# Kernel tuning notes

Hardware: AMD Instinct MI355X
Metric: run time of the kernel (lower is better)

## Reference

```python
import jax, jax.numpy as jnp
import numpy as np

N = 512
NODE_IN = 64
NODE_OUT = 64
ED_IN = 32
ED_OUT = 32
STATE = 80  # must satisfy 2*NODE_IN + ED_IN == 2*STATE
SLOPE = 0.1
EPS = 1e-5


def setup_inputs() -> dict:
    key = jax.random.key(0)
    ks = jax.random.split(key, 10)
    def lin(k, out_f, in_f):
        return jax.random.normal(k, (out_f, in_f), jnp.float32) / np.sqrt(in_f).astype(np.float32)
    x = jax.random.normal(ks[0], (N, NODE_IN), jnp.float32)
    edge_attr = jax.random.normal(ks[1], (N * N, ED_IN), jnp.float32)
    mask = jax.random.randint(ks[2], (N * N, 1), 0, 2).astype(jnp.int32)
    return {
        "x": x,
        "edge_attr": edge_attr,
        "mask": mask,
        "W_nu": lin(ks[3], NODE_OUT, NODE_IN),
        "b_nu": jnp.zeros((NODE_OUT,), jnp.float32),
        "W_h2": lin(ks[4], STATE, 2 * STATE),
        "b_h2": jnp.zeros((STATE,), jnp.float32),
        "W_eo": lin(ks[5], ED_OUT, STATE),
        "b_eo": jnp.zeros((ED_OUT,), jnp.float32),
        "e_vec": jax.random.normal(ks[6], (2 * NODE_OUT + ED_OUT,), jnp.float32) * 0.1,
        "bn_n_w": jnp.ones((NODE_OUT,), jnp.float32),
        "bn_n_b": jnp.zeros((NODE_OUT,), jnp.float32),
        "bn_e_w": jnp.ones((ED_OUT,), jnp.float32),
        "bn_e_b": jnp.zeros((ED_OUT,), jnp.float32),
    }


def _lrelu(v):
    return jax.nn.leaky_relu(v, SLOPE)


def _bn(v, w, b):
    # BatchNorm1d, training-mode (batch stats, biased variance)
    mu = v.mean(axis=0)
    var = v.var(axis=0)
    return (v - mu) / jnp.sqrt(var + EPS) * w + b


def reference(x, edge_attr, mask, W_nu, b_nu, W_h2, b_h2, W_eo, b_eo, e_vec,
              bn_n_w, bn_n_b, bn_e_w, bn_e_b):
    n = x.shape[0]
    m = mask.astype(x.dtype)  # [N*N, 1]
    # triplet_e[i*N+j] = [x_i, edge_attr_{ij}, x_j]
    src = jnp.repeat(x, n, axis=0)          # [N*N, NODE_IN]
    dst = jnp.tile(x, (n, 1))               # [N*N, NODE_IN]
    triplet_e = jnp.concatenate([src, edge_attr, dst], axis=-1)  # [N*N, 2*STATE]
    # NOTE: ed_trans_layer / ed_hidden_1 outputs are dead code in the source.
    h = _lrelu(triplet_e @ W_h2.T + b_h2)                 # [N*N, STATE]
    new_edge_attr = _lrelu(h @ W_eo.T + b_eo)             # [N*N, ED_OUT]
    new_edge_attr = new_edge_attr * m
    xn = _lrelu(x @ W_nu.T + b_nu)                        # [N, NODE_OUT]
    triplet_n = jnp.concatenate(
        [jnp.repeat(xn, n, axis=0), new_edge_attr, jnp.tile(xn, (n, 1))], axis=-1
    ).reshape(n, n, 2 * NODE_OUT + ED_OUT)
    scores = _lrelu(jnp.einsum("ijd,d->ij", triplet_n, e_vec))  # [N, N]
    att = jax.nn.softmax(scores, axis=1)
    att = (att.reshape(n * n, 1) * m).reshape(n, n)
    # dropout disabled (deterministic / eval)
    new_x = att @ xn                                       # [N, NODE_OUT]
    new_x = _bn(new_x, bn_n_w, bn_n_b)
    new_edge_attr = _bn(new_edge_attr, bn_e_w, bn_e_b)
    return new_x, new_edge_attr
```

## Files before the change

### kernel.cpp

```cpp
#include <hip/hip_runtime.h>

#define SLOPE 0.1f
#define EPS 1e-5f

typedef __bf16 bf16x8 __attribute__((ext_vector_type(8)));
typedef unsigned short u16x8 __attribute__((ext_vector_type(8)));
typedef float f32x4 __attribute__((ext_vector_type(4)));
typedef unsigned u32x4 __attribute__((ext_vector_type(4)));

#define WS_ESC 0
#define WS_ESH 32
#define WS_A 64
#define WS_B 576
#define WS_XN 1088
#define WS_NEWX 33856
#define WS_P1B 66624
#define WS_SC 107584
#define WS_PART 369728
#define WSH_WB 804992
#define WSH_WB2 810112
#define WSH_WO 812672
#define WSH_XB 815744
#define WSH_NE 848512

__device__ __forceinline__ float lrelu(float v) { return v > 0.f ? v : SLOPE * v; }
__device__ __forceinline__ unsigned short f2bf(float f) {
  unsigned x = __float_as_uint(f);
  return (unsigned short)((x + 0x7fffu + ((x >> 16) & 1u)) >> 16);
}
__device__ __forceinline__ float bf2f(unsigned short u) {
  return __uint_as_float(((unsigned)u) << 16);
}

__global__ void __launch_bounds__(256) k1(const float* __restrict__ x,
                                          const float* __restrict__ W_nu,
                                          const float* __restrict__ b_nu,
                                          const float* __restrict__ W_h2,
                                          const float* __restrict__ b_h2,
                                          const float* __restrict__ W_eo,
                                          const float* __restrict__ ev,
                                          float* ws) {
  int blk = blockIdx.x;
  int tid = threadIdx.x;
  unsigned short* wsh = (unsigned short*)ws;
  if (blk < 128) {
    __shared__ float wlds[64 * 65];
#pragma unroll
    for (int it = 0; it < 16; it++) {
      int idx = it * 256 + tid;
      wlds[(idx >> 6) * 65 + (idx & 63)] = W_nu[idx];
    }
    int gid = blk * 256 + tid;
    wsh[WSH_XB + gid] = f2bf(x[gid]);
    ws[WS_PART + gid] = 0.f;
    if (gid < 5120) {
      int c = gid / 2560, r = gid - c * 2560;
      int t = r >> 9, l = (r >> 3) & 63, jj = r & 7;
      int n = t * 16 + (l & 15);
      int k = (l >> 4) * 8 + jj + c * 32;
      wsh[WSH_WB + gid] = f2bf(W_h2[n * 160 + 64 + k]);
    } else if (gid < 7680) {
      int idx = gid - 5120;
      int t = idx >> 9, l = (idx >> 3) & 63, jj = idx & 7;
      int n = t * 16 + (l & 15);
      int k = (l >> 4) * 8 + jj;
      wsh[WSH_WB2 + idx] = f2bf(W_h2[n * 160 + 128 + k]);
    } else if (gid < 10752) {
      int idx = gid - 7680;
      int t2 = idx / 1536, r2 = idx - t2 * 1536;
      int s = r2 >> 9, l = (r2 >> 3) & 63, jj = r2 & 7;
      int n = t2 * 16 + (l & 15);
      int k = s * 32 + (l >> 4) * 8 + jj;
      wsh[WSH_WO + idx] = (k < 80) ? f2bf(W_eo[n * 80 + k]) : (unsigned short)0;
    }
    __syncthreads();
    int i = blk * 4 + (tid >> 6);
    int c = tid & 63;
    float acc = b_nu[c];
    const float* xr = x + i * 64;
#pragma unroll 8
    for (int k = 0; k < 64; k++) acc += xr[k] * wlds[c * 65 + k];
    float xnv = lrelu(acc);
    ws[WS_XN + i * 64 + c] = xnv;
    float va = xnv * ev[c];
    float vb = xnv * ev[96 + c];
#pragma unroll
    for (int off = 32; off >= 1; off >>= 1) {
      va += __shfl_xor(va, off, 64);
      vb += __shfl_xor(vb, off, 64);
    }
    if (c == 0) { ws[WS_A + i] = va; ws[WS_B + i] = vb; }
  } else {
    int b2 = blk - 128;
    int bm = b2 & 7, bn = b2 >> 3;
    int wave = tid >> 6, lane = tid & 63;
    int c16 = lane & 15, q = lane >> 4;
    int n = bn * 16 + c16;
    const float* wrow = W_h2 + n * 160;
    int mrow = bm * 64 + wave * 16 + c16;
    bf16x8 bfr[2], afr[2];
#pragma unroll
    for (int ks = 0; ks < 2; ks++) {
      const float* bs = wrow + ks * 32 + q * 8;
      const float* as = x + mrow * 64 + ks * 32 + q * 8;
      u16x8 ub, ua;
#pragma unroll
      for (int jj = 0; jj < 8; jj++) { ub[jj] = f2bf(bs[jj]); ua[jj] = f2bf(as[jj]); }
      bfr[ks] = __builtin_bit_cast(bf16x8, ub);
      afr[ks] = __builtin_bit_cast(bf16x8, ua);
    }
    float bias = b_h2[n];
    f32x4 acc = {bias, bias, bias, bias};
    acc = __builtin_amdgcn_mfma_f32_16x16x32_bf16(afr[0], bfr[0], acc, 0, 0, 0);
    acc = __builtin_amdgcn_mfma_f32_16x16x32_bf16(afr[1], bfr[1], acc, 0, 0, 0);
#pragma unroll
    for (int r = 0; r < 4; r++) {
      int mm = bm * 64 + wave * 16 + q * 4 + r;
      ws[WS_P1B + mm * 80 + n] = acc[r];
    }
  }
}

__global__ void __launch_bounds__(256) k2(const float* __restrict__ ea,
                                          const int* __restrict__ mask,
                                          const float* __restrict__ b_eo,
                                          const float* __restrict__ ev,
                                          float* ws) {
  __shared__ unsigned short wlds[10752];
  __shared__ unsigned short ht[64 * 104];
  __shared__ float p1s[80];
  __shared__ float wred[2][4][32];
  int tid = threadIdx.x;
  int w = tid >> 6, lane = tid & 63;
  int c16 = lane & 15, q = lane >> 4;
  int blk = blockIdx.x;
  int i = blk >> 3, j0 = (blk & 7) << 6;
  int jb = j0 + w * 16;
  const unsigned short* wsh = (const unsigned short*)ws;
  unsigned* ne32 = (unsigned*)((unsigned short*)ws + WSH_NE);

#pragma unroll
  for (int it = 0; it < 6; it++) {
    int idx = it * 256 + tid;
    if (idx < 1344) *(u16x8*)&wlds[idx * 8] = *(const u16x8*)(wsh + WSH_WB + idx * 8);
  }
  if (tid < 80) p1s[tid] = ws[WS_P1B + i * 80 + tid];
  float beo0 = b_eo[c16], beo1 = b_eo[16 + c16];
  float eve0 = ev[64 + c16], eve1 = ev[80 + c16];
  float a_i = ws[WS_A + i];
  __syncthreads();

  bf16x8 af0;
  {
    const float* src = ea + (i * 512 + jb + c16) * 32 + q * 8;
    u16x8 u;
#pragma unroll
    for (int jj = 0; jj < 8; jj++) u[jj] = f2bf(src[jj]);
    af0 = __builtin_bit_cast(bf16x8, u);
  }
  bf16x8 af1 = __builtin_bit_cast(
      bf16x8, *(const u16x8*)(wsh + WSH_XB + (jb + c16) * 64 + q * 8));
  bf16x8 af2 = __builtin_bit_cast(
      bf16x8, *(const u16x8*)(wsh + WSH_XB + (jb + c16) * 64 + 32 + q * 8));

  f32x4 acc[5];
#pragma unroll
  for (int t = 0; t < 5; t++) {
    float p1v = p1s[t * 16 + c16];
    acc[t] = {p1v, p1v, p1v, p1v};
  }
#pragma unroll
  for (int t = 0; t < 5; t++) {
    bf16x8 wb = __builtin_bit_cast(bf16x8, *(const u16x8*)&wlds[t * 512 + lane * 8]);
    acc[t] = __builtin_amdgcn_mfma_f32_16x16x32_bf16(af0, wb, acc[t], 0, 0, 0);
  }
#pragma unroll
  for (int t = 0; t < 5; t++) {
    bf16x8 wb =
        __builtin_bit_cast(bf16x8, *(const u16x8*)&wlds[2560 + t * 512 + lane * 8]);
    acc[t] = __builtin_amdgcn_mfma_f32_16x16x32_bf16(af1, wb, acc[t], 0, 0, 0);
  }
#pragma unroll
  for (int t = 0; t < 5; t++) {
    bf16x8 wb =
        __builtin_bit_cast(bf16x8, *(const u16x8*)&wlds[5120 + t * 512 + lane * 8]);
    acc[t] = __builtin_amdgcn_mfma_f32_16x16x32_bf16(af2, wb, acc[t], 0, 0, 0);
  }
#pragma unroll
  for (int t = 0; t < 5; t++)
#pragma unroll
    for (int r = 0; r < 4; r++)
      ht[(w * 16 + q * 4 + r) * 104 + t * 16 + c16] = f2bf(lrelu(acc[t][r]));

  f32x4 acc2[2] = {{0.f, 0.f, 0.f, 0.f}, {0.f, 0.f, 0.f, 0.f}};
  int hrow = w * 16 + c16;
#pragma unroll
  for (int s = 0; s < 3; s++) {
    int kk = s * 32 + q * 8;
    u16x8 hb = {0, 0, 0, 0, 0, 0, 0, 0};
    if (kk < 80) hb = *(const u16x8*)&ht[hrow * 104 + kk];
    bf16x8 ha = __builtin_bit_cast(bf16x8, hb);
    bf16x8 wo0 =
        __builtin_bit_cast(bf16x8, *(const u16x8*)&wlds[7680 + s * 512 + lane * 8]);
    bf16x8 wo1 = __builtin_bit_cast(
        bf16x8, *(const u16x8*)&wlds[7680 + 1536 + s * 512 + lane * 8]);
    acc2[0] = __builtin_amdgcn_mfma_f32_16x16x32_bf16(ha, wo0, acc2[0], 0, 0, 0);
    acc2[1] = __builtin_amdgcn_mfma_f32_16x16x32_bf16(ha, wo1, acc2[1], 0, 0, 0);
  }

  float scs0 = 0.f, scss0 = 0.f, scs1 = 0.f, scss1 = 0.f;
  float se[4];
#pragma unroll
  for (int r = 0; r < 4; r++) {
    int m = i * 512 + jb + q * 4 + r;
    float mf = mask[m] ? 1.f : 0.f;
    float v0 = lrelu(acc2[0][r] + beo0) * mf;
    float v1 = lrelu(acc2[1][r] + beo1) * mf;
    scs0 += v0; scss0 += v0 * v0;
    scs1 += v1; scss1 += v1 * v1;
    ne32[m * 16 + c16] = (unsigned)f2bf(v0) | ((unsigned)f2bf(v1) << 16);
    float s = v0 * eve0 + v1 * eve1;
#pragma unroll
    for (int off = 8; off >= 1; off >>= 1) s += __shfl_xor(s, off, 64);
    se[r] = s;
  }
  if (c16 < 4) {
    int j = jb + q * 4 + c16;
    float s = (c16 == 0) ? se[0] : (c16 == 1) ? se[1] : (c16 == 2) ? se[2] : se[3];
    ws[WS_SC + i * 512 + j] = lrelu(a_i + ws[WS_B + j] + s);
  }
  scs0 += __shfl_xor(scs0, 16, 64); scs0 += __shfl_xor(scs0, 32, 64);
  scss0 += __shfl_xor(scss0, 16, 64); scss0 += __shfl_xor(scss0, 32, 64);
  scs1 += __shfl_xor(scs1, 16, 64); scs1 += __shfl_xor(scs1, 32, 64);
  scss1 += __shfl_xor(scss1, 16, 64); scss1 += __shfl_xor(scss1, 32, 64);
  if (q == 0) {
    wred[0][w][c16] = scs0; wred[0][w][16 + c16] = scs1;
    wred[1][w][c16] = scss0; wred[1][w][16 + c16] = scss1;
  }
  __syncthreads();
  if (tid < 64) {
    int half = tid >> 5, col = tid & 31;
    float v = wred[half][0][col] + wred[half][1][col] + wred[half][2][col] +
              wred[half][3][col];
    atomicAdd(&ws[WS_PART + (blk >> 3) * 64 + tid], v);
  }
}

__global__ void __launch_bounds__(512) k3(const int* __restrict__ mask,
                                          const float* __restrict__ bn_e_w,
                                          const float* __restrict__ bn_e_b,
                                          float* ws) {
  __shared__ float att[512];
  __shared__ float red[8];
  __shared__ float nx[8][64];
  int i = blockIdx.x, tid = threadIdx.x;
  int wave = tid >> 6, lane = tid & 63;
  if (i == 512) {
    int g = tid >> 6, c = tid & 63;
    float a = 0.f;
    for (int s = g; s < 512; s += 8) a += ws[WS_PART + s * 64 + c];
    nx[g][c] = a;
    __syncthreads();
    if (tid < 64) {
      float t = 0.f;
#pragma unroll
      for (int g2 = 0; g2 < 8; g2++) t += nx[g2][tid];
      att[tid] = t;
    }
    __syncthreads();
    if (tid < 32) {
      float mean = att[tid] * (1.f / 262144.f);
      float var = att[tid + 32] * (1.f / 262144.f) - mean * mean;
      float s = bn_e_w[tid] * rsqrtf(fmaxf(var, 0.f) + EPS);
      ws[WS_ESC + tid] = s;
      ws[WS_ESH + tid] = bn_e_b[tid] - mean * s;
    }
    return;
  }
  float p = __expf(ws[WS_SC + i * 512 + tid]);
  float sm = p;
#pragma unroll
  for (int off = 32; off >= 1; off >>= 1) sm += __shfl_xor(sm, off, 64);
  if (lane == 0) red[wave] = sm;
  __syncthreads();
  float tot = red[0] + red[1] + red[2] + red[3] + red[4] + red[5] + red[6] + red[7];
  att[tid] = p * (1.f / tot) * (mask[i * 512 + tid] ? 1.f : 0.f);
  __syncthreads();
  int c = lane;
  const float* xn = ws + WS_XN;
  float accv = 0.f;
#pragma unroll 4
  for (int u = 0; u < 64; u++) {
    int j = wave * 64 + u;
    accv += att[j] * xn[j * 64 + c];
  }
  nx[wave][c] = accv;
  __syncthreads();
  if (tid < 64) {
    float s = 0.f;
#pragma unroll
    for (int w = 0; w < 8; w++) s += nx[w][tid];
    ws[WS_NEWX + i * 64 + tid] = s;
  }
}

__global__ void __launch_bounds__(256) k5(const float* __restrict__ bn_n_w,
                                          const float* __restrict__ bn_n_b,
                                          const float* __restrict__ ws,
                                          float* __restrict__ out) {
  int blk = blockIdx.x, tid = threadIdx.x;
  if (blk < 8) {
    __shared__ float s1[4][64], s2[4][64], scl[64], sh[64];
    int c = tid & 63, g = tid >> 6;
    float a = 0.f, b = 0.f;
#pragma unroll 4
    for (int u = 0; u < 128; u++) {
      float v = ws[WS_NEWX + (g * 128 + u) * 64 + c];
      a += v;
      b += v * v;
    }
    s1[g][c] = a;
    s2[g][c] = b;
    __syncthreads();
    if (tid < 64) {
      float sum = s1[0][tid] + s1[1][tid] + s1[2][tid] + s1[3][tid];
      float ssq = s2[0][tid] + s2[1][tid] + s2[2][tid] + s2[3][tid];
      float mean = sum * (1.f / 512.f);
      float var = ssq * (1.f / 512.f) - mean * mean;
      float s = bn_n_w[tid] * rsqrtf(fmaxf(var, 0.f) + EPS);
      scl[tid] = s;
      sh[tid] = bn_n_b[tid] - mean * s;
    }
    __syncthreads();
#pragma unroll 4
    for (int u = 0; u < 16; u++) {
      int idx = blk * 4096 + u * 256 + tid;
      int c2 = idx & 63;
      out[idx] = ws[WS_NEWX + idx] * scl[c2] + sh[c2];
    }
  } else {
    const unsigned* ne32 = (const unsigned*)((const unsigned short*)ws + WSH_NE);
    int b4 = ((blk - 8) * 256 + tid) * 4;
    u32x4 raw = *(const u32x4*)(ne32 + b4);
    int e32 = (b4 >> 4) * 32;
    int cb = b4 & 15;
    f32x4 esc0 = *(const f32x4*)(ws + WS_ESC + cb);
    f32x4 esc1 = *(const f32x4*)(ws + WS_ESC + 16 + cb);
    f32x4 esh0 = *(const f32x4*)(ws + WS_ESH + cb);
    f32x4 esh1 = *(const f32x4*)(ws + WS_ESH + 16 + cb);
    f32x4 lo, hi;
#pragma unroll
    for (int u = 0; u < 4; u++) {
      lo[u] = bf2f((unsigned short)(raw[u] & 0xffffu)) * esc0[u] + esh0[u];
      hi[u] = bf2f((unsigned short)(raw[u] >> 16)) * esc1[u] + esh1[u];
    }
    float* oe = out + 32768;
    *(f32x4*)(oe + e32 + cb) = lo;
    *(f32x4*)(oe + e32 + 16 + cb) = hi;
  }
}

extern "C" void kernel_launch(void* const* d_in, const int* in_sizes, int n_in,
                              void* d_out, int out_size, void* d_ws, size_t ws_size,
                              hipStream_t stream) {
  const float* x = (const float*)d_in[0];
  const float* ea = (const float*)d_in[1];
  const int* mask = (const int*)d_in[2];
  const float* Wnu = (const float*)d_in[3];
  const float* bnu = (const float*)d_in[4];
  const float* Wh2 = (const float*)d_in[5];
  const float* bh2 = (const float*)d_in[6];
  const float* Weo = (const float*)d_in[7];
  const float* beo = (const float*)d_in[8];
  const float* ev = (const float*)d_in[9];
  const float* bnw = (const float*)d_in[10];
  const float* bnb = (const float*)d_in[11];
  const float* bew = (const float*)d_in[12];
  const float* beb = (const float*)d_in[13];
  float* ws = (float*)d_ws;
  float* out = (float*)d_out;

  k1<<<168, 256, 0, stream>>>(x, Wnu, bnu, Wh2, bh2, Weo, ev, ws);
  k2<<<4096, 256, 0, stream>>>(ea, mask, beo, ev, ws);
  k3<<<513, 512, 0, stream>>>(mask, bew, beb, ws);
  k5<<<4104, 256, 0, stream>>>(bnw, bnb, ws, out);
}
```

Measured before the change: 159.9 us.

## Fuse edge BatchNorm output into attention kernel and vectorize edge/mask loads

Moves the edge BatchNorm statistics finalization and the normalized-edge write from the separate stats block and the 4096 extra k5 blocks into every k3 block. Each k3 block now redundantly reduces the partial sums and then writes its own row of normalized edge attributes, which leaves k5 handling only node BN. In k2, the edge_attr and mask loads become vector loads. The cost is redundant reduction work in each of 512 blocks, traded for fewer blocks and cheaper edge-path memory access.

```diff
diff --git a/kernel.cpp b/kernel.cpp
--- a/kernel.cpp
+++ b/kernel.cpp
@@ -153,15 +153,20 @@
   bf16x8 af0;
   {
     const float* src = ea + (i * 512 + jb + c16) * 32 + q * 8;
+    f32x4 e0 = *(const f32x4*)src;
+    f32x4 e1 = *(const f32x4*)(src + 4);
     u16x8 u;
 #pragma unroll
-    for (int jj = 0; jj < 8; jj++) u[jj] = f2bf(src[jj]);
+    for (int jj = 0; jj < 4; jj++) { u[jj] = f2bf(e0[jj]); u[4 + jj] = f2bf(e1[jj]); }
     af0 = __builtin_bit_cast(bf16x8, u);
   }
   bf16x8 af1 = __builtin_bit_cast(
       bf16x8, *(const u16x8*)(wsh + WSH_XB + (jb + c16) * 64 + q * 8));
   bf16x8 af2 = __builtin_bit_cast(
       bf16x8, *(const u16x8*)(wsh + WSH_XB + (jb + c16) * 64 + 32 + q * 8));
+  int4 mk = *(const int4*)(mask + i * 512 + jb + q * 4);
+  int mkv[4];
+  mkv[0] = mk.x; mkv[1] = mk.y; mkv[2] = mk.z; mkv[3] = mk.w;
 
   f32x4 acc[5];
 #pragma unroll
@@ -213,7 +218,7 @@
 #pragma unroll
   for (int r = 0; r < 4; r++) {
     int m = i * 512 + jb + q * 4 + r;
-    float mf = mask[m] ? 1.f : 0.f;
+    float mf = mkv[r] ? 1.f : 0.f;
     float v0 = lrelu(acc2[0][r] + beo0) * mf;
     float v1 = lrelu(acc2[1][r] + beo1) * mf;
     scs0 += v0; scss0 += v0 * v0;
@@ -249,34 +254,36 @@
 __global__ void __launch_bounds__(512) k3(const int* __restrict__ mask,
                                           const float* __restrict__ bn_e_w,
                                           const float* __restrict__ bn_e_b,
-                                          float* ws) {
+                                          float* ws, float* __restrict__ out) {
   __shared__ float att[512];
   __shared__ float red[8];
   __shared__ float nx[8][64];
+  __shared__ __attribute__((aligned(16))) float escsh[64];
   int i = blockIdx.x, tid = threadIdx.x;
   int wave = tid >> 6, lane = tid & 63;
-  if (i == 512) {
-    int g = tid >> 6, c = tid & 63;
+
+  {
     float a = 0.f;
-    for (int s = g; s < 512; s += 8) a += ws[WS_PART + s * 64 + c];
-    nx[g][c] = a;
-    __syncthreads();
-    if (tid < 64) {
-      float t = 0.f;
-#pragma unroll
-      for (int g2 = 0; g2 < 8; g2++) t += nx[g2][tid];
-      att[tid] = t;
-    }
-    __syncthreads();
-    if (tid < 32) {
-      float mean = att[tid] * (1.f / 262144.f);
-      float var = att[tid + 32] * (1.f / 262144.f) - mean * mean;
-      float s = bn_e_w[tid] * rsqrtf(fmaxf(var, 0.f) + EPS);
-      ws[WS_ESC + tid] = s;
-      ws[WS_ESH + tid] = bn_e_b[tid] - mean * s;
-    }
-    return;
-  }
+    for (int s = wave; s < 512; s += 8) a += ws[WS_PART + s * 64 + lane];
+    nx[wave][lane] = a;
+  }
+  __syncthreads();
+  if (tid < 64) {
+    float t = 0.f;
+#pragma unroll
+    for (int g2 = 0; g2 < 8; g2++) t += nx[g2][tid];
+    att[tid] = t;
+  }
+  __syncthreads();
+  if (tid < 32) {
+    float mean = att[tid] * (1.f / 262144.f);
+    float var = att[tid + 32] * (1.f / 262144.f) - mean * mean;
+    float s = bn_e_w[tid] * rsqrtf(fmaxf(var, 0.f) + EPS);
+    escsh[tid] = s;
+    escsh[32 + tid] = bn_e_b[tid] - mean * s;
+  }
+  __syncthreads();
+
   float p = __expf(ws[WS_SC + i * 512 + tid]);
   float sm = p;
 #pragma unroll
@@ -286,21 +293,43 @@
   float tot = red[0] + red[1] + red[2] + red[3] + red[4] + red[5] + red[6] + red[7];
   att[tid] = p * (1.f / tot) * (mask[i * 512 + tid] ? 1.f : 0.f);
   __syncthreads();
-  int c = lane;
   const float* xn = ws + WS_XN;
   float accv = 0.f;
 #pragma unroll 4
   for (int u = 0; u < 64; u++) {
     int j = wave * 64 + u;
-    accv += att[j] * xn[j * 64 + c];
-  }
-  nx[wave][c] = accv;
+    accv += att[j] * xn[j * 64 + lane];
+  }
+  nx[wave][lane] = accv;
   __syncthreads();
   if (tid < 64) {
     float s = 0.f;
 #pragma unroll
-    for (int w = 0; w < 8; w++) s += nx[w][tid];
+    for (int w2 = 0; w2 < 8; w2++) s += nx[w2][tid];
     ws[WS_NEWX + i * 64 + tid] = s;
+  }
+
+  const unsigned* ner =
+      (const unsigned*)((const unsigned short*)ws + WSH_NE) + i * 8192;
+  float* oe = out + 32768 + i * 16384;
+  int cb = (tid & 3) << 2;
+  f32x4 esc0 = *(const f32x4*)&escsh[cb];
+  f32x4 esc1 = *(const f32x4*)&escsh[16 + cb];
+  f32x4 esh0 = *(const f32x4*)&escsh[32 + cb];
+  f32x4 esh1 = *(const f32x4*)&escsh[48 + cb];
+#pragma unroll
+  for (int it = 0; it < 4; it++) {
+    int b4 = it * 2048 + tid * 4;
+    u32x4 raw = *(const u32x4*)(ner + b4);
+    int e32 = (b4 >> 4) * 32;
+    f32x4 lo, hi;
+#pragma unroll
+    for (int u = 0; u < 4; u++) {
+      lo[u] = bf2f((unsigned short)(raw[u] & 0xffffu)) * esc0[u] + esh0[u];
+      hi[u] = bf2f((unsigned short)(raw[u] >> 16)) * esc1[u] + esh1[u];
+    }
+    *(f32x4*)(oe + e32 + cb) = lo;
+    *(f32x4*)(oe + e32 + 16 + cb) = hi;
   }
 }
 
@@ -309,54 +338,33 @@
                                           const float* __restrict__ ws,
                                           float* __restrict__ out) {
   int blk = blockIdx.x, tid = threadIdx.x;
-  if (blk < 8) {
-    __shared__ float s1[4][64], s2[4][64], scl[64], sh[64];
-    int c = tid & 63, g = tid >> 6;
-    float a = 0.f, b = 0.f;
+  __shared__ float s1[4][64], s2[4][64], scl[64], sh[64];
+  int c = tid & 63, g = tid >> 6;
+  float a = 0.f, b = 0.f;
 #pragma unroll 4
-    for (int u = 0; u < 128; u++) {
-      float v = ws[WS_NEWX + (g * 128 + u) * 64 + c];
-      a += v;
-      b += v * v;
-    }
-    s1[g][c] = a;
-    s2[g][c] = b;
-    __syncthreads();
-    if (tid < 64) {
-      float sum = s1[0][tid] + s1[1][tid] + s1[2][tid] + s1[3][tid];
-      float ssq = s2[0][tid] + s2[1][tid] + s2[2][tid] + s2[3][tid];
-      float mean = sum * (1.f / 512.f);
-      float var = ssq * (1.f / 512.f) - mean * mean;
-      float s = bn_n_w[tid] * rsqrtf(fmaxf(var, 0.f) + EPS);
-      scl[tid] = s;
-      sh[tid] = bn_n_b[tid] - mean * s;
-    }
-    __syncthreads();
+  for (int u = 0; u < 128; u++) {
+    float v = ws[WS_NEWX + (g * 128 + u) * 64 + c];
+    a += v;
+    b += v * v;
+  }
+  s1[g][c] = a;
+  s2[g][c] = b;
+  __syncthreads();
+  if (tid < 64) {
+    float sum = s1[0][tid] + s1[1][tid] + s1[2][tid] + s1[3][tid];
+    float ssq = s2[0][tid] + s2[1][tid] + s2[2][tid] + s2[3][tid];
+    float mean = sum * (1.f / 512.f);
+    float var = ssq * (1.f / 512.f) - mean * mean;
+    float s = bn_n_w[tid] * rsqrtf(fmaxf(var, 0.f) + EPS);
+    scl[tid] = s;
+    sh[tid] = bn_n_b[tid] - mean * s;
+  }
+  __syncthreads();
 #pragma unroll 4
-    for (int u = 0; u < 16; u++) {
-      int idx = blk * 4096 + u * 256 + tid;
-      int c2 = idx & 63;
-      out[idx] = ws[WS_NEWX + idx] * scl[c2] + sh[c2];
-    }
-  } else {
-    const unsigned* ne32 = (const unsigned*)((const unsigned short*)ws + WSH_NE);
-    int b4 = ((blk - 8) * 256 + tid) * 4;
-    u32x4 raw = *(const u32x4*)(ne32 + b4);
-    int e32 = (b4 >> 4) * 32;
-    int cb = b4 & 15;
-    f32x4 esc0 = *(const f32x4*)(ws + WS_ESC + cb);
-    f32x4 esc1 = *(const f32x4*)(ws + WS_ESC + 16 + cb);
-    f32x4 esh0 = *(const f32x4*)(ws + WS_ESH + cb);
-    f32x4 esh1 = *(const f32x4*)(ws + WS_ESH + 16 + cb);
-    f32x4 lo, hi;
-#pragma unroll
-    for (int u = 0; u < 4; u++) {
-      lo[u] = bf2f((unsigned short)(raw[u] & 0xffffu)) * esc0[u] + esh0[u];
-      hi[u] = bf2f((unsigned short)(raw[u] >> 16)) * esc1[u] + esh1[u];
-    }
-    float* oe = out + 32768;
-    *(f32x4*)(oe + e32 + cb) = lo;
-    *(f32x4*)(oe + e32 + 16 + cb) = hi;
+  for (int u = 0; u < 16; u++) {
+    int idx = blk * 4096 + u * 256 + tid;
+    int c2 = idx & 63;
+    out[idx] = ws[WS_NEWX + idx] * scl[c2] + sh[c2];
   }
 }
 
@@ -382,6 +390,6 @@
 
   k1<<<168, 256, 0, stream>>>(x, Wnu, bnu, Wh2, bh2, Weo, ev, ws);
   k2<<<4096, 256, 0, stream>>>(ea, mask, beo, ev, ws);
-  k3<<<513, 512, 0, stream>>>(mask, bew, beb, ws);
-  k5<<<4104, 256, 0, stream>>>(bnw, bnb, ws, out);
-}
+  k3<<<512, 512, 0, stream>>>(mask, bew, beb, ws, out);
+  k5<<<8, 256, 0, stream>>>(bnw, bnb, ws, out);
+}
```

Result: slower. 167.1 us (+4.5%).
